# Kernel optimization log

Hardware: AMD Instinct MI355X
Metric: run time of the kernel (lower is better)

Reference implementation:

```python
import jax, jax.numpy as jnp
import numpy as np

B, T = 4096, 20
X_DIM, Z_DIM, H_DIM = 256, 128, 512
ZL, HL = 64, 64
D = X_DIM + Z_DIM  # 384, size of A


def _linear_params(key, out_f, in_f):
    kw, kb = jax.random.split(key)
    bound = 1.0 / np.sqrt(in_f)
    W = jax.random.uniform(kw, (out_f, in_f), minval=-bound, maxval=bound, dtype=jnp.float32)
    b = jax.random.uniform(kb, (out_f,), minval=-bound, maxval=bound, dtype=jnp.float32)
    return W, b


def setup_inputs() -> dict:
    key = jax.random.key(0)
    ks = jax.random.split(key, 12)
    x = jax.random.normal(ks[0], (B, T, X_DIM), dtype=jnp.float32)
    h_in = jax.random.normal(ks[1], (B, T, HL), dtype=jnp.float32)
    z_in = jax.random.normal(ks[2], (B, T, ZL), dtype=jnp.float32)
    A = jax.random.normal(ks[3], (D, D), dtype=jnp.float32) / np.sqrt(D)
    # Pz_xh_mean_forward: LinearUnit(x+h -> h), LinearUnit(h -> z)
    Wm1, bm1 = _linear_params(ks[4], H_DIM, X_DIM + H_DIM)
    Wm2, bm2 = _linear_params(ks[5], Z_DIM, H_DIM)
    # Pz_xh_logvar_forward: same shapes
    Wv1, bv1 = _linear_params(ks[6], H_DIM, X_DIM + H_DIM)
    Wv2, bv2 = _linear_params(ks[7], Z_DIM, H_DIM)
    # phi_xz_forward: LinearUnit(x+z -> 2h)
    Wphi, bphi = _linear_params(ks[8], 2 * H_DIM, X_DIM + Z_DIM)
    # LSTMCell(2h -> h), torch layout: gates order i, f, g, o
    W_ih, b_ih = _linear_params(ks[9], 4 * H_DIM, 2 * H_DIM)
    W_hh, b_hh = _linear_params(ks[10], 4 * H_DIM, H_DIM)
    return dict(x=x, h_in=h_in, z_in=z_in, A=A,
                Wm1=Wm1, bm1=bm1, Wm2=Wm2, bm2=bm2,
                Wv1=Wv1, bv1=bv1, Wv2=Wv2, bv2=bv2,
                Wphi=Wphi, bphi=bphi,
                W_ih=W_ih, W_hh=W_hh, b_ih=b_ih, b_hh=b_hh)


def _forward(x, h_in, z_in, A, Wm1, bm1, Wm2, bm2, Wv1, bv1, Wv2, bv2,
             Wphi, bphi, W_ih, W_hh, b_ih, b_hh):
    lrelu = lambda v: jax.nn.leaky_relu(v, 0.2)

    def step(carry, x_t):
        h, c = carry  # [B, H] each
        xh = jnp.concatenate([x_t, h], axis=1)                       # [B, X+H]
        mean = lrelu(lrelu(xh @ Wm1.T + bm1) @ Wm2.T + bm2)          # [B, Z]
        logvar = lrelu(lrelu(xh @ Wv1.T + bv1) @ Wv2.T + bv2)        # [B, Z]
        z = mean  # eval mode: reparameterize_gaussian returns the mean
        xz = jnp.concatenate([x_t, z], axis=1)                       # [B, D]
        agg = xz @ A.T  # == matmul(A, xz.T).T                       # [B, D]
        phi = jax.nn.softplus(lrelu(agg @ Wphi.T + bphi))            # [B, 2H]
        gates = phi @ W_ih.T + b_ih + h @ W_hh.T + b_hh              # [B, 4H]
        i, f, g, o = jnp.split(gates, 4, axis=1)
        c_new = jax.nn.sigmoid(f) * c + jax.nn.sigmoid(i) * jnp.tanh(g)
        h_new = jax.nn.sigmoid(o) * jnp.tanh(c_new)
        # h_out records h BEFORE the update (as in the torch loop)
        return (h_new, c_new), (z, mean, logvar, h, h_new)

    h0 = jnp.zeros((x.shape[0], H_DIM), dtype=x.dtype)
    c0 = jnp.zeros((x.shape[0], H_DIM), dtype=x.dtype)
    xT = jnp.swapaxes(x, 0, 1)  # [T, B, X]
    _, (z, mean, logvar, h_out, h_lo) = jax.lax.scan(step, (h0, c0), xT)
    to_bt = lambda a: jnp.swapaxes(a, 0, 1)  # [B, T, *]
    return (to_bt(z), to_bt(mean), to_bt(logvar), to_bt(h_out), to_bt(h_lo))


def reference(x, h_in, z_in, A, Wm1, bm1, Wm2, bm2, Wv1, bv1, Wv2, bv2,
              Wphi, bphi, W_ih, W_hh, b_ih, b_hh):
    return _forward(x, h_in, z_in, A, Wm1, bm1, Wm2, bm2, Wv1, bv1, Wv2, bv2,
                    Wphi, bphi, W_ih, W_hh, b_ih, b_hh)
```

## Files before the change

kernel.cpp:

```cpp
#include <hip/hip_runtime.h>
#include <math.h>

constexpr int B_ = 4096;
constexpr int T_ = 20;
constexpr int XD = 256;
constexpr int ZD = 128;
constexpr int HD = 512;
constexpr int DD = 384;

using short8 = __attribute__((ext_vector_type(8))) short;
using bf16x8 = __attribute__((ext_vector_type(8))) __bf16;
using f32x4  = __attribute__((ext_vector_type(4))) float;

__device__ __forceinline__ float lrelu_f(float v) { return v > 0.f ? v : 0.2f * v; }
__device__ __forceinline__ float softplus_f(float v) {
    return log1pf(expf(-fabsf(v))) + fmaxf(v, 0.f);
}
__device__ __forceinline__ float sigmoid_f(float v) { return 1.f / (1.f + expf(-v)); }

__device__ __forceinline__ unsigned short f2b(float f) {
    unsigned u = __builtin_bit_cast(unsigned, f);
    u += 0x7fff + ((u >> 16) & 1);
    return (unsigned short)(u >> 16);
}

__device__ __forceinline__ f32x4 mfma16(short8 a, short8 b, f32x4 c) {
    return __builtin_amdgcn_mfma_f32_16x16x32_bf16(
        __builtin_bit_cast(bf16x8, a), __builtin_bit_cast(bf16x8, b), c, 0, 0, 0);
}

__device__ __forceinline__ void load_lds16(const unsigned short* g, unsigned short* l) {
    __builtin_amdgcn_global_load_lds(
        (const __attribute__((address_space(1))) unsigned int*)g,
        (__attribute__((address_space(3))) unsigned int*)l,
        16, 0, 0);
}

template <int LPT>
__device__ __forceinline__ void vmwait(int rem) {
    if (rem >= 2) {
        if constexpr (LPT == 4)      asm volatile("s_waitcnt vmcnt(8)" ::: "memory");
        else if constexpr (LPT == 3) asm volatile("s_waitcnt vmcnt(6)" ::: "memory");
        else                         asm volatile("s_waitcnt vmcnt(4)" ::: "memory");
    } else if (rem == 1) {
        if constexpr (LPT == 4)      asm volatile("s_waitcnt vmcnt(4)" ::: "memory");
        else if constexpr (LPT == 3) asm volatile("s_waitcnt vmcnt(3)" ::: "memory");
        else                         asm volatile("s_waitcnt vmcnt(2)" ::: "memory");
    } else {
        asm volatile("s_waitcnt vmcnt(0)" ::: "memory");
    }
}

template <int MT>
__device__ __forceinline__ void gemm_core(
    const unsigned short* A1, int lda1, int K1,
    const unsigned short* A2, int lda2, int K2,
    const unsigned short* W1, int ldw1,
    const unsigned short* W2, int ldw2,
    int bm, int bn,
    unsigned short* As, unsigned short* Bs,
    f32x4 (&acc)[MT / 32][4])
{
    constexpr int MI   = MT / 32;
    constexpr int WRS  = MT / 2;
    constexpr int NA   = MT / 64;
    constexpr int LPT  = NA + 2;
    constexpr int ABUF = MT * 32;

    const int tid  = threadIdx.x;
    const int lane = tid & 63;
    const int wave = tid >> 6;
    const int wr = wave >> 1, wc = wave & 1;
    const int fr = lane & 15, fg = lane >> 4;
    const int cswz = fg ^ ((fr >> 1) & 3);

    const int r0 = tid >> 2,          c0 = (tid & 3) ^ ((r0 >> 1) & 3);
    const int r1 = (256 + tid) >> 2,  c1 = ((256 + tid) & 3) ^ ((r1 >> 1) & 3);

    const int n1 = K1 / 32;
    const int nt = n1 + K2 / 32;

    auto stage = [&](int i, int buf) {
        const unsigned short* Ag;
        const unsigned short* Wg;
        int lda, ldw, kb;
        if (i < n1) { Ag = A1; Wg = W1; lda = lda1; ldw = ldw1; kb = i * 32; }
        else        { Ag = A2; Wg = W2; lda = lda2; ldw = ldw2; kb = (i - n1) * 32; }
        unsigned short* lA = As + buf * ABUF + wave * 512;
        unsigned short* lB = Bs + buf * 4096 + wave * 512;
        load_lds16(Ag + (size_t)(bm + r0) * lda + kb + c0 * 8, lA);
        if constexpr (NA == 2)
            load_lds16(Ag + (size_t)(bm + r1) * lda + kb + c1 * 8, lA + 2048);
        load_lds16(Wg + (size_t)(bn + r0) * ldw + kb + c0 * 8, lB);
        load_lds16(Wg + (size_t)(bn + r1) * ldw + kb + c1 * 8, lB + 2048);
    };

    auto compute = [&](int buf) {
        const unsigned short* Ab_ = As + buf * ABUF;
        const unsigned short* Bb_ = Bs + buf * 4096;
        short8 af[MI], bv[4];
#pragma unroll
        for (int mi = 0; mi < MI; ++mi)
            af[mi] = *reinterpret_cast<const short8*>(Ab_ + (wr * WRS + mi * 16 + fr) * 32 + cswz * 8);
#pragma unroll
        for (int ni = 0; ni < 4; ++ni)
            bv[ni] = *reinterpret_cast<const short8*>(Bb_ + (wc * 64 + ni * 16 + fr) * 32 + cswz * 8);
#pragma unroll
        for (int mi = 0; mi < MI; ++mi)
#pragma unroll
            for (int ni = 0; ni < 4; ++ni)
                acc[mi][ni] = mfma16(af[mi], bv[ni], acc[mi][ni]);
    };

    stage(0, 0);
    if (1 < nt) stage(1, 1);
    if (2 < nt) stage(2, 2);
    {
        int rem = (nt - 1 < 2) ? (nt - 1) : 2;
        vmwait<LPT>(rem);
    }
    __builtin_amdgcn_s_barrier();

    int buf = 0;
    for (int i = 0; i < nt; ++i) {
        compute(buf);
        if (i + 1 < nt) {
            asm volatile("" ::: "memory");
            __builtin_amdgcn_s_barrier();
            if (i + 3 < nt) stage(i + 3, buf);
            int rem = nt - (i + 2);
            if (rem > 2) rem = 2;
            vmwait<LPT>(rem);
            __builtin_amdgcn_s_barrier();
            buf = (buf == 2) ? 0 : buf + 1;
        }
    }
}

template <int ACT, int MT, int NMASK, int NSHIFT>
__global__ __launch_bounds__(256) void k_gemm_act(
    const unsigned short* __restrict__ A1, int lda1, int K1,
    const unsigned short* __restrict__ A2, int lda2, int K2,
    const unsigned short* __restrict__ W1, int ldw1,
    const unsigned short* __restrict__ W2, int ldw2,
    const float* __restrict__ bias,
    unsigned short* __restrict__ DB, int lddb)
{
    __shared__ unsigned short As[3 * MT * 32];
    __shared__ unsigned short Bs[3 * 4096];
    const int id = blockIdx.x;
    const int bm = (id >> NSHIFT) * MT, bn = (id & NMASK) * 128;
    f32x4 acc[MT / 32][4] = {};
    gemm_core<MT>(A1, lda1, K1, A2, lda2, K2, W1, ldw1, W2, ldw2, bm, bn, As, Bs, acc);

    constexpr int MI = MT / 32, WRS = MT / 2;
    const int tid = threadIdx.x, lane = tid & 63, wave = tid >> 6;
    const int wr = wave >> 1, wc = wave & 1, fr = lane & 15, rg = lane >> 4;
    float bb[4];
#pragma unroll
    for (int ni = 0; ni < 4; ++ni)
        bb[ni] = bias ? bias[bn + wc * 64 + ni * 16 + fr] : 0.f;
#pragma unroll
    for (int mi = 0; mi < MI; ++mi)
#pragma unroll
        for (int r = 0; r < 4; ++r) {
            const int row = bm + wr * WRS + mi * 16 + rg * 4 + r;
#pragma unroll
            for (int ni = 0; ni < 4; ++ni) {
                float v = acc[mi][ni][r] + bb[ni];
                if (ACT == 1) v = lrelu_f(v);
                else if (ACT == 2) v = softplus_f(lrelu_f(v));
                DB[(size_t)row * lddb + (bn + wc * 64 + ni * 16 + fr)] = f2b(v);
            }
        }
}

__global__ __launch_bounds__(256) void k_meanphi(
    const unsigned short* __restrict__ uslot,
    const unsigned short* __restrict__ xb,
    const unsigned short* __restrict__ Wm2b,
    const unsigned short* __restrict__ Wcb,
    const float* __restrict__ bm2,
    const float* __restrict__ bphi,
    float* __restrict__ oz, float* __restrict__ om,
    unsigned short* __restrict__ phib)
{
    __shared__ unsigned short As[3 * 64 * 32];
    __shared__ unsigned short Bs[3 * 4096];
    __shared__ unsigned short meanL[64 * 136];

    const int id = blockIdx.x;
    const int bm = (id >> 3) * 64, bn = (id & 7) * 128;
    const int tid = threadIdx.x, lane = tid & 63, wave = tid >> 6;
    const int wr = wave >> 1, wc = wave & 1, fr = lane & 15, fg = lane >> 4, rg = lane >> 4;
    const int cswz = fg ^ ((fr >> 1) & 3);
    const int r0 = tid >> 2,          c0 = (tid & 3) ^ ((r0 >> 1) & 3);
    const int r1 = (256 + tid) >> 2,  c1 = ((256 + tid) & 3) ^ ((r1 >> 1) & 3);

    {
        f32x4 macc[2][4] = {};
        gemm_core<64>(uslot, 1024, 512, uslot, 1024, 0,
                      Wm2b, 512, Wm2b, 512, bm, 0, As, Bs, macc);
        float mb[4];
#pragma unroll
        for (int ni = 0; ni < 4; ++ni)
            mb[ni] = bm2[wc * 64 + ni * 16 + fr];
#pragma unroll
        for (int mi = 0; mi < 2; ++mi)
#pragma unroll
            for (int r = 0; r < 4; ++r) {
                const int rowl = wr * 32 + mi * 16 + rg * 4 + r;
#pragma unroll
                for (int ni = 0; ni < 4; ++ni) {
                    const int col = wc * 64 + ni * 16 + fr;
                    const float v = lrelu_f(macc[mi][ni][r] + mb[ni]);
                    meanL[rowl * 136 + col] = f2b(v);
                    if (bn == 0) {
                        const size_t o = (size_t)(bm + rowl) * (T_ * ZD) + col;
                        oz[o] = v; om[o] = v;
                    }
                }
            }
    }
    __syncthreads();

    f32x4 acc[2][4] = {};
    gemm_core<64>(xb, XD, XD, xb, XD, 0,
                  Wcb, DD, Wcb, DD, bm, bn, As, Bs, acc);
    __syncthreads();

    {
        const unsigned short* WG = Wcb + XD;
        auto stageB = [&](int i, int buf) {
            unsigned short* lB = Bs + buf * 4096 + wave * 512;
            load_lds16(WG + (size_t)(bn + r0) * DD + i * 32 + c0 * 8, lB);
            load_lds16(WG + (size_t)(bn + r1) * DD + i * 32 + c1 * 8, lB + 2048);
        };
        stageB(0, 0); stageB(1, 1); stageB(2, 2);
        vmwait<2>(2);
        __builtin_amdgcn_s_barrier();
        int buf = 0;
        for (int i = 0; i < 4; ++i) {
            short8 af[2], bv[4];
#pragma unroll
            for (int mi = 0; mi < 2; ++mi)
                af[mi] = *reinterpret_cast<const short8*>(
                    meanL + (wr * 32 + mi * 16 + fr) * 136 + i * 32 + fg * 8);
#pragma unroll
            for (int ni = 0; ni < 4; ++ni)
                bv[ni] = *reinterpret_cast<const short8*>(
                    Bs + buf * 4096 + (wc * 64 + ni * 16 + fr) * 32 + cswz * 8);
#pragma unroll
            for (int mi = 0; mi < 2; ++mi)
#pragma unroll
                for (int ni = 0; ni < 4; ++ni)
                    acc[mi][ni] = mfma16(af[mi], bv[ni], acc[mi][ni]);
            if (i + 1 < 4) {
                asm volatile("" ::: "memory");
                __builtin_amdgcn_s_barrier();
                if (i + 3 < 4) stageB(i + 3, buf);
                int rem = 4 - (i + 2);
                if (rem > 2) rem = 2;
                vmwait<2>(rem);
                __builtin_amdgcn_s_barrier();
                buf = (buf == 2) ? 0 : buf + 1;
            }
        }
    }

    float pb[4];
#pragma unroll
    for (int ni = 0; ni < 4; ++ni)
        pb[ni] = bphi[bn + wc * 64 + ni * 16 + fr];
#pragma unroll
    for (int mi = 0; mi < 2; ++mi)
#pragma unroll
        for (int r = 0; r < 4; ++r) {
            const int row = bm + wr * 32 + mi * 16 + rg * 4 + r;
#pragma unroll
            for (int ni = 0; ni < 4; ++ni) {
                const float v = softplus_f(lrelu_f(acc[mi][ni][r] + pb[ni]));
                phib[(size_t)row * 1024 + (bn + wc * 64 + ni * 16 + fr)] = f2b(v);
            }
        }
}

__global__ __launch_bounds__(256) void k_logvar_all(
    const unsigned short* __restrict__ umuvall,
    const unsigned short* __restrict__ Wv2b,
    const float* __restrict__ bv2,
    float* __restrict__ out_lv)
{
    __shared__ unsigned short As[3 * 64 * 32];
    __shared__ unsigned short Bs[3 * 4096];
    const int bm = blockIdx.x * 64;
    f32x4 acc[2][4] = {};
    gemm_core<64>(umuvall + 512, 1024, 512, umuvall + 512, 1024, 0,
                  Wv2b, 512, Wv2b, 512, bm, 0, As, Bs, acc);

    const int tid = threadIdx.x, lane = tid & 63, wave = tid >> 6;
    const int wr = wave >> 1, wc = wave & 1, fr = lane & 15, rg = lane >> 4;
    float bb[4];
#pragma unroll
    for (int ni = 0; ni < 4; ++ni)
        bb[ni] = bv2[wc * 64 + ni * 16 + fr];
#pragma unroll
    for (int mi = 0; mi < 2; ++mi)
#pragma unroll
        for (int r = 0; r < 4; ++r) {
            const int row = bm + wr * 32 + mi * 16 + rg * 4 + r;
            const int t = row >> 12, b = row & (B_ - 1);
#pragma unroll
            for (int ni = 0; ni < 4; ++ni) {
                const int col = wc * 64 + ni * 16 + fr;
                out_lv[(size_t)b * (T_ * ZD) + (size_t)t * ZD + col] =
                    lrelu_f(acc[mi][ni][r] + bb[ni]);
            }
        }
}

__global__ __launch_bounds__(256) void k_gates_lstm(
    const unsigned short* __restrict__ phib,
    const unsigned short* __restrict__ hbin,
    const unsigned short* __restrict__ Wih,
    const unsigned short* __restrict__ Whh,
    const float* __restrict__ br,
    float* __restrict__ c,
    unsigned short* __restrict__ hbout,
    float* __restrict__ ohl,
    float* __restrict__ oh_next)
{
    __shared__ unsigned short As[3 * 128 * 32];
    __shared__ unsigned short Bs[3 * 4096];
    const int id = blockIdx.x;
    const int sid = (id & 7) * 64 + (id >> 3);
    const int bm = (sid >> 4) * 128, bn = (sid & 15) * 128;
    f32x4 acc[4][4] = {};
    gemm_core<128>(phib, 1024, 1024, hbin, 512, 512, Wih, 1024, Whh, 512, bm, bn, As, Bs, acc);

    const int tid = threadIdx.x, lane = tid & 63, wave = tid >> 6;
    const int wr = wave >> 1, wc = wave & 1, fr = lane & 15, rg = lane >> 4;
    const int n = ((bn + wc * 64) >> 6) * 16 + fr;
    float bb[4];
#pragma unroll
    for (int ni = 0; ni < 4; ++ni)
        bb[ni] = br[bn + wc * 64 + ni * 16 + fr];
#pragma unroll
    for (int mi = 0; mi < 4; ++mi)
#pragma unroll
        for (int r = 0; r < 4; ++r) {
            const int row = bm + wr * 64 + mi * 16 + rg * 4 + r;
            const size_t idx = (size_t)row * HD + n;
            const float gi = acc[mi][0][r] + bb[0];
            const float gf = acc[mi][1][r] + bb[1];
            const float gg = acc[mi][2][r] + bb[2];
            const float go = acc[mi][3][r] + bb[3];
            const float co = c[idx];
            const float cn = sigmoid_f(gf) * co + sigmoid_f(gi) * tanhf(gg);
            const float hn = sigmoid_f(go) * tanhf(cn);
            c[idx] = cn;
            hbout[idx] = f2b(hn);
            const size_t ob = (size_t)row * (T_ * HD) + n;
            ohl[ob] = hn;
            if (oh_next) oh_next[ob] = hn;
        }
}

__global__ __launch_bounds__(256) void k_gemm_plain(
    const unsigned short* __restrict__ A1, int lda1, int K1,
    const unsigned short* __restrict__ W1, int ldw1,
    unsigned short* __restrict__ DB, int lddb)
{
    __shared__ unsigned short As[3 * 128 * 32];
    __shared__ unsigned short Bs[3 * 4096];
    const int bm = blockIdx.y * 128, bn = blockIdx.x * 128;
    f32x4 acc[4][4] = {};
    gemm_core<128>(A1, lda1, K1, A1, lda1, 0, W1, ldw1, W1, ldw1, bm, bn, As, Bs, acc);

    const int tid = threadIdx.x, lane = tid & 63, wave = tid >> 6;
    const int wr = wave >> 1, wc = wave & 1, fr = lane & 15, rg = lane >> 4;
#pragma unroll
    for (int mi = 0; mi < 4; ++mi)
#pragma unroll
        for (int r = 0; r < 4; ++r) {
            const int row = bm + wr * 64 + mi * 16 + rg * 4 + r;
#pragma unroll
            for (int ni = 0; ni < 4; ++ni) {
                const int col = bn + wc * 64 + ni * 16 + fr;
                DB[(size_t)row * lddb + col] = f2b(acc[mi][ni][r]);
            }
        }
}

__global__ __launch_bounds__(256) void init_state(
    float* __restrict__ c, unsigned short* __restrict__ hb,
    float* __restrict__ oh0)
{
    const int i = blockIdx.x * 256 + threadIdx.x;
    c[i] = 0.f; hb[i] = 0;
    const int b = i >> 9, nn = i & 511;
    oh0[(size_t)b * (T_ * HD) + nn] = 0.f;
}

__global__ __launch_bounds__(256) void f32_to_bf16(
    const float* __restrict__ src, unsigned short* __restrict__ dst, int n4)
{
    const int i = blockIdx.x * 256 + threadIdx.x;
    if (i >= n4) return;
    float4 v = reinterpret_cast<const float4*>(src)[i];
    ushort4 o;
    o.x = f2b(v.x); o.y = f2b(v.y); o.z = f2b(v.z); o.w = f2b(v.w);
    reinterpret_cast<ushort4*>(dst)[i] = o;
}

__global__ __launch_bounds__(256) void conv_x_all(
    const float* __restrict__ x, unsigned short* __restrict__ xball)
{
    const int i = blockIdx.x * 256 + threadIdx.x;
    const int d = i & 63;
    const int bt = i >> 6;
    const int b = bt / T_, t = bt % T_;
    float4 v = reinterpret_cast<const float4*>(x)[i];
    ushort4 o;
    o.x = f2b(v.x); o.y = f2b(v.y); o.z = f2b(v.z); o.w = f2b(v.w);
    reinterpret_cast<ushort4*>(xball)[((size_t)t * B_ + b) * (XD / 4) + d] = o;
}

__global__ __launch_bounds__(256) void prep_wu(
    const float* __restrict__ Wm1, const float* __restrict__ Wv1,
    unsigned short* __restrict__ Wub)
{
    const int k = blockIdx.x * 256 + threadIdx.x;
    const int nrow = blockIdx.y;
    const float v = nrow < 512 ? Wm1[nrow * 768 + k] : Wv1[(nrow - 512) * 768 + k];
    Wub[nrow * 768 + k] = f2b(v);
}

__global__ __launch_bounds__(256) void prep_wg(
    const float* __restrict__ Wih, const float* __restrict__ Whh,
    unsigned short* __restrict__ Wrih, unsigned short* __restrict__ Wrhh)
{
    const int cc = blockIdx.y;
    const int gate = (cc >> 4) & 3;
    const int n = ((cc >> 6) << 4) + (cc & 15);
    const int orig = gate * 512 + n;
    const int kk = blockIdx.x * 256 + threadIdx.x;
    if (kk < 1024) Wrih[(size_t)cc * 1024 + kk] = f2b(Wih[(size_t)orig * 1024 + kk]);
    else           Wrhh[(size_t)cc * 512 + (kk - 1024)] = f2b(Whh[(size_t)orig * 512 + (kk - 1024)]);
}

__global__ __launch_bounds__(256) void prep_at(
    const float* __restrict__ A, unsigned short* __restrict__ At)
{
    const int i = blockIdx.x * 256 + threadIdx.x;
    const int k = i / DD, j = i % DD;
    At[(size_t)k * DD + j] = f2b(A[(size_t)j * DD + k]);
}

__global__ __launch_bounds__(256) void prep_bias(
    const float* __restrict__ bm1, const float* __restrict__ bv1,
    const float* __restrict__ bih, const float* __restrict__ bhh,
    float* __restrict__ bu, float* __restrict__ br)
{
    const int i = blockIdx.x * 256 + threadIdx.x;
    if (i < 1024) {
        bu[i] = i < 512 ? bm1[i] : bv1[i - 512];
    } else if (i >= 2048) {
        const int cb = i - 2048;
        const int gate = (cb >> 4) & 3;
        const int n = ((cb >> 6) << 4) + (cb & 15);
        const int orig = gate * 512 + n;
        br[cb] = bih[orig] + bhh[orig];
    }
}

extern "C" void kernel_launch(void* const* d_in, const int* in_sizes, int n_in,
                              void* d_out, int out_size, void* d_ws, size_t ws_size,
                              hipStream_t stream)
{
    const float* x    = (const float*)d_in[0];
    const float* A    = (const float*)d_in[3];
    const float* Wm1  = (const float*)d_in[4];
    const float* bm1  = (const float*)d_in[5];
    const float* Wm2  = (const float*)d_in[6];
    const float* bm2  = (const float*)d_in[7];
    const float* Wv1  = (const float*)d_in[8];
    const float* bv1  = (const float*)d_in[9];
    const float* Wv2  = (const float*)d_in[10];
    const float* bv2  = (const float*)d_in[11];
    const float* Wphi = (const float*)d_in[12];
    const float* bphi = (const float*)d_in[13];
    const float* W_ih = (const float*)d_in[14];
    const float* W_hh = (const float*)d_in[15];
    const float* b_ih = (const float*)d_in[16];
    const float* b_hh = (const float*)d_in[17];

    float* out = (float*)d_out;
    float* out_z    = out;
    float* out_mean = out_z + (size_t)B_ * T_ * ZD;
    float* out_lv   = out_mean + (size_t)B_ * T_ * ZD;
    float* out_hout = out_lv + (size_t)B_ * T_ * ZD;
    float* out_hlo  = out_hout + (size_t)B_ * T_ * HD;

    char* wp = (char*)d_ws;
    auto alloc_f = [&](size_t n) { float* p = (float*)wp; wp += n * sizeof(float); return p; };
    auto alloc_b = [&](size_t n) { unsigned short* p = (unsigned short*)wp; wp += n * sizeof(unsigned short); return p; };

    float* c = alloc_f((size_t)B_ * HD);
    unsigned short* hb0     = alloc_b((size_t)B_ * HD);
    unsigned short* hb1     = alloc_b((size_t)B_ * HD);
    unsigned short* xball   = alloc_b((size_t)T_ * B_ * XD);
    unsigned short* umuvall = alloc_b((size_t)T_ * B_ * 1024);
    unsigned short* phib    = alloc_b((size_t)B_ * 1024);

    unsigned short* Wub   = alloc_b((size_t)1024 * 768);
    unsigned short* Wm2b  = alloc_b((size_t)ZD * HD);
    unsigned short* Wv2b  = alloc_b((size_t)ZD * HD);
    unsigned short* Atb   = alloc_b((size_t)DD * DD);
    unsigned short* Wphib = alloc_b((size_t)1024 * DD);
    unsigned short* Wcb   = alloc_b((size_t)1024 * DD);
    unsigned short* Wrih  = alloc_b((size_t)2048 * 1024);
    unsigned short* Wrhh  = alloc_b((size_t)2048 * 512);

    float* bu = alloc_f(1024);
    float* br = alloc_f(2048);

    const dim3 blk(256);

    init_state<<<dim3(B_ * HD / 256), blk, 0, stream>>>(c, hb0, out_hout);
    conv_x_all<<<dim3(B_ * T_ * XD / 4 / 256), blk, 0, stream>>>(x, xball);
    prep_wu<<<dim3(3, 1024), blk, 0, stream>>>(Wm1, Wv1, Wub);
    f32_to_bf16<<<dim3(ZD * HD / 4 / 256), blk, 0, stream>>>(Wm2, Wm2b, ZD * HD / 4);
    f32_to_bf16<<<dim3(ZD * HD / 4 / 256), blk, 0, stream>>>(Wv2, Wv2b, ZD * HD / 4);
    prep_wg<<<dim3(6, 2048), blk, 0, stream>>>(W_ih, W_hh, Wrih, Wrhh);
    prep_bias<<<dim3(16), blk, 0, stream>>>(bm1, bv1, b_ih, b_hh, bu, br);
    prep_at<<<dim3(DD * DD / 256), blk, 0, stream>>>(A, Atb);
    f32_to_bf16<<<dim3(1024 * DD / 4 / 256), blk, 0, stream>>>(Wphi, Wphib, 1024 * DD / 4);
    k_gemm_plain<<<dim3(DD / 128, 1024 / 128), blk, 0, stream>>>(
        Wphib, DD, DD, Atb, DD, Wcb, DD);

    for (int t = 0; t < T_; ++t) {
        unsigned short* hbt = (t & 1) ? hb1 : hb0;
        unsigned short* hbn = (t & 1) ? hb0 : hb1;
        const unsigned short* xb = xball + (size_t)t * B_ * XD;
        unsigned short* uslot = umuvall + (size_t)t * B_ * 1024;

        k_gemm_act<1, 64, 7, 3><<<dim3(512), blk, 0, stream>>>(
            xb, XD, XD, hbt, HD, HD,
            Wub, XD + HD, Wub + XD, XD + HD,
            bu, uslot, 1024);

        k_meanphi<<<dim3(512), blk, 0, stream>>>(
            uslot, xb, Wm2b, Wcb, bm2, bphi,
            out_z + (size_t)t * ZD, out_mean + (size_t)t * ZD, phib);

        k_gates_lstm<<<dim3(512), blk, 0, stream>>>(
            phib, hbt, Wrih, Wrhh, br,
            c, hbn,
            out_hlo + (size_t)t * HD,
            (t + 1 < T_) ? out_hout + (size_t)(t + 1) * HD : nullptr);
    }

    k_logvar_all<<<dim3(T_ * B_ / 64), blk, 0, stream>>>(
        umuvall, Wv2b, bv2, out_lv);
}
```

Baseline: 2.065 ms.

## Widen LSTM gate GEMM tile to 256 rows and merge prep kernels into one launch

```diff
diff --git a/kernel.cpp b/kernel.cpp
--- a/kernel.cpp
+++ b/kernel.cpp
@@ -39,11 +39,13 @@
 template <int LPT>
 __device__ __forceinline__ void vmwait(int rem) {
     if (rem >= 2) {
-        if constexpr (LPT == 4)      asm volatile("s_waitcnt vmcnt(8)" ::: "memory");
+        if constexpr (LPT == 6)      asm volatile("s_waitcnt vmcnt(12)" ::: "memory");
+        else if constexpr (LPT == 4) asm volatile("s_waitcnt vmcnt(8)" ::: "memory");
         else if constexpr (LPT == 3) asm volatile("s_waitcnt vmcnt(6)" ::: "memory");
         else                         asm volatile("s_waitcnt vmcnt(4)" ::: "memory");
     } else if (rem == 1) {
-        if constexpr (LPT == 4)      asm volatile("s_waitcnt vmcnt(4)" ::: "memory");
+        if constexpr (LPT == 6)      asm volatile("s_waitcnt vmcnt(6)" ::: "memory");
+        else if constexpr (LPT == 4) asm volatile("s_waitcnt vmcnt(4)" ::: "memory");
         else if constexpr (LPT == 3) asm volatile("s_waitcnt vmcnt(3)" ::: "memory");
         else                         asm volatile("s_waitcnt vmcnt(2)" ::: "memory");
     } else {
@@ -137,6 +139,83 @@
     }
 }
 
+__device__ __forceinline__ void gemm_core_wide(
+    const unsigned short* A1, int lda1, int K1,
+    const unsigned short* A2, int lda2, int K2,
+    const unsigned short* W1, int ldw1,
+    const unsigned short* W2, int ldw2,
+    int bm, int bn,
+    unsigned short* As, unsigned short* Bs,
+    f32x4 (&acc)[8][4])
+{
+    const int tid  = threadIdx.x;
+    const int lane = tid & 63;
+    const int wave = tid >> 6;
+    const int wr = wave >> 1, wc = wave & 1;
+    const int fr = lane & 15, fg = lane >> 4;
+    const int cswz = fg ^ ((fr >> 1) & 3);
+
+    const int rr = tid >> 2;
+    const int cc_ = (tid & 3) ^ ((rr >> 1) & 3);
+
+    const int n1 = K1 / 32;
+    const int nt = n1 + K2 / 32;
+
+    auto stage = [&](int i, int buf) {
+        const unsigned short* Ag;
+        const unsigned short* Wg;
+        int lda, ldw, kb;
+        if (i < n1) { Ag = A1; Wg = W1; lda = lda1; ldw = ldw1; kb = i * 32; }
+        else        { Ag = A2; Wg = W2; lda = lda2; ldw = ldw2; kb = (i - n1) * 32; }
+        unsigned short* lA = As + buf * 8192 + wave * 512;
+        unsigned short* lB = Bs + buf * 4096 + wave * 512;
+#pragma unroll
+        for (int j = 0; j < 4; ++j)
+            load_lds16(Ag + (size_t)(bm + j * 64 + rr) * lda + kb + cc_ * 8, lA + j * 2048);
+#pragma unroll
+        for (int j = 0; j < 2; ++j)
+            load_lds16(Wg + (size_t)(bn + j * 64 + rr) * ldw + kb + cc_ * 8, lB + j * 2048);
+    };
+
+    auto compute = [&](int buf) {
+        const unsigned short* Ab_ = As + buf * 8192;
+        const unsigned short* Bb_ = Bs + buf * 4096;
+        short8 af[8], bv[4];
+#pragma unroll
+        for (int mi = 0; mi < 8; ++mi)
+            af[mi] = *reinterpret_cast<const short8*>(Ab_ + (wr * 128 + mi * 16 + fr) * 32 + cswz * 8);
+#pragma unroll
+        for (int ni = 0; ni < 4; ++ni)
+            bv[ni] = *reinterpret_cast<const short8*>(Bb_ + (wc * 64 + ni * 16 + fr) * 32 + cswz * 8);
+#pragma unroll
+        for (int mi = 0; mi < 8; ++mi)
+#pragma unroll
+            for (int ni = 0; ni < 4; ++ni)
+                acc[mi][ni] = mfma16(af[mi], bv[ni], acc[mi][ni]);
+    };
+
+    stage(0, 0);
+    stage(1, 1);
+    stage(2, 2);
+    vmwait<6>(2);
+    __builtin_amdgcn_s_barrier();
+
+    int buf = 0;
+    for (int i = 0; i < nt; ++i) {
+        compute(buf);
+        if (i + 1 < nt) {
+            asm volatile("" ::: "memory");
+            __builtin_amdgcn_s_barrier();
+            if (i + 3 < nt) stage(i + 3, buf);
+            int rem = nt - (i + 2);
+            if (rem > 2) rem = 2;
+            vmwait<6>(rem);
+            __builtin_amdgcn_s_barrier();
+            buf = (buf == 2) ? 0 : buf + 1;
+        }
+    }
+}
+
 template <int ACT, int MT, int NMASK, int NSHIFT>
 __global__ __launch_bounds__(256) void k_gemm_act(
     const unsigned short* __restrict__ A1, int lda1, int K1,
@@ -330,13 +409,13 @@
     float* __restrict__ ohl,
     float* __restrict__ oh_next)
 {
-    __shared__ unsigned short As[3 * 128 * 32];
+    __shared__ unsigned short As[3 * 8192];
     __shared__ unsigned short Bs[3 * 4096];
     const int id = blockIdx.x;
-    const int sid = (id & 7) * 64 + (id >> 3);
-    const int bm = (sid >> 4) * 128, bn = (sid & 15) * 128;
-    f32x4 acc[4][4] = {};
-    gemm_core<128>(phib, 1024, 1024, hbin, 512, 512, Wih, 1024, Whh, 512, bm, bn, As, Bs, acc);
+    const int sid = (id & 7) * 32 + (id >> 3);
+    const int bm = (sid >> 4) * 256, bn = (sid & 15) * 128;
+    f32x4 acc[8][4] = {};
+    gemm_core_wide(phib, 1024, 1024, hbin, 512, 512, Wih, 1024, Whh, 512, bm, bn, As, Bs, acc);
 
     const int tid = threadIdx.x, lane = tid & 63, wave = tid >> 6;
     const int wr = wave >> 1, wc = wave & 1, fr = lane & 15, rg = lane >> 4;
@@ -346,10 +425,10 @@
     for (int ni = 0; ni < 4; ++ni)
         bb[ni] = br[bn + wc * 64 + ni * 16 + fr];
 #pragma unroll
-    for (int mi = 0; mi < 4; ++mi)
+    for (int mi = 0; mi < 8; ++mi)
 #pragma unroll
         for (int r = 0; r < 4; ++r) {
-            const int row = bm + wr * 64 + mi * 16 + rg * 4 + r;
+            const int row = bm + wr * 128 + mi * 16 + rg * 4 + r;
             const size_t idx = (size_t)row * HD + n;
             const float gi = acc[mi][0][r] + bb[0];
             const float gf = acc[mi][1][r] + bb[1];
@@ -392,85 +471,98 @@
         }
 }
 
-__global__ __launch_bounds__(256) void init_state(
-    float* __restrict__ c, unsigned short* __restrict__ hb,
-    float* __restrict__ oh0)
-{
-    const int i = blockIdx.x * 256 + threadIdx.x;
-    c[i] = 0.f; hb[i] = 0;
-    const int b = i >> 9, nn = i & 511;
-    oh0[(size_t)b * (T_ * HD) + nn] = 0.f;
-}
-
-__global__ __launch_bounds__(256) void f32_to_bf16(
-    const float* __restrict__ src, unsigned short* __restrict__ dst, int n4)
-{
-    const int i = blockIdx.x * 256 + threadIdx.x;
-    if (i >= n4) return;
-    float4 v = reinterpret_cast<const float4*>(src)[i];
-    ushort4 o;
-    o.x = f2b(v.x); o.y = f2b(v.y); o.z = f2b(v.z); o.w = f2b(v.w);
-    reinterpret_cast<ushort4*>(dst)[i] = o;
-}
-
-__global__ __launch_bounds__(256) void conv_x_all(
-    const float* __restrict__ x, unsigned short* __restrict__ xball)
-{
-    const int i = blockIdx.x * 256 + threadIdx.x;
-    const int d = i & 63;
-    const int bt = i >> 6;
-    const int b = bt / T_, t = bt % T_;
-    float4 v = reinterpret_cast<const float4*>(x)[i];
-    ushort4 o;
-    o.x = f2b(v.x); o.y = f2b(v.y); o.z = f2b(v.z); o.w = f2b(v.w);
-    reinterpret_cast<ushort4*>(xball)[((size_t)t * B_ + b) * (XD / 4) + d] = o;
-}
-
-__global__ __launch_bounds__(256) void prep_wu(
-    const float* __restrict__ Wm1, const float* __restrict__ Wv1,
-    unsigned short* __restrict__ Wub)
-{
-    const int k = blockIdx.x * 256 + threadIdx.x;
-    const int nrow = blockIdx.y;
-    const float v = nrow < 512 ? Wm1[nrow * 768 + k] : Wv1[(nrow - 512) * 768 + k];
-    Wub[nrow * 768 + k] = f2b(v);
-}
-
-__global__ __launch_bounds__(256) void prep_wg(
+constexpr int SG0 = 8192;
+constexpr int SG1 = SG0 + 20480;
+constexpr int SG2 = SG1 + 3072;
+constexpr int SG3 = SG2 + 64;
+constexpr int SG4 = SG3 + 64;
+constexpr int SG5 = SG4 + 384;
+constexpr int SG6 = SG5 + 12288;
+constexpr int SG7 = SG6 + 576;
+constexpr int SG8 = SG7 + 16;
+
+__global__ __launch_bounds__(256) void prep_all(
+    const float* __restrict__ x,
+    const float* __restrict__ A,
+    const float* __restrict__ Wm1, const float* __restrict__ bm1,
+    const float* __restrict__ Wm2,
+    const float* __restrict__ Wv1, const float* __restrict__ bv1,
+    const float* __restrict__ Wv2,
+    const float* __restrict__ Wphi,
     const float* __restrict__ Wih, const float* __restrict__ Whh,
-    unsigned short* __restrict__ Wrih, unsigned short* __restrict__ Wrhh)
-{
-    const int cc = blockIdx.y;
-    const int gate = (cc >> 4) & 3;
-    const int n = ((cc >> 6) << 4) + (cc & 15);
-    const int orig = gate * 512 + n;
-    const int kk = blockIdx.x * 256 + threadIdx.x;
-    if (kk < 1024) Wrih[(size_t)cc * 1024 + kk] = f2b(Wih[(size_t)orig * 1024 + kk]);
-    else           Wrhh[(size_t)cc * 512 + (kk - 1024)] = f2b(Whh[(size_t)orig * 512 + (kk - 1024)]);
-}
-
-__global__ __launch_bounds__(256) void prep_at(
-    const float* __restrict__ A, unsigned short* __restrict__ At)
-{
-    const int i = blockIdx.x * 256 + threadIdx.x;
-    const int k = i / DD, j = i % DD;
-    At[(size_t)k * DD + j] = f2b(A[(size_t)j * DD + k]);
-}
-
-__global__ __launch_bounds__(256) void prep_bias(
-    const float* __restrict__ bm1, const float* __restrict__ bv1,
     const float* __restrict__ bih, const float* __restrict__ bhh,
+    float* __restrict__ c, unsigned short* __restrict__ hb0,
+    float* __restrict__ oh0,
+    unsigned short* __restrict__ xball,
+    unsigned short* __restrict__ Wub,
+    unsigned short* __restrict__ Wm2b, unsigned short* __restrict__ Wv2b,
+    unsigned short* __restrict__ Wphib,
+    unsigned short* __restrict__ Wrih, unsigned short* __restrict__ Wrhh,
+    unsigned short* __restrict__ Atb,
     float* __restrict__ bu, float* __restrict__ br)
 {
-    const int i = blockIdx.x * 256 + threadIdx.x;
-    if (i < 1024) {
-        bu[i] = i < 512 ? bm1[i] : bv1[i - 512];
-    } else if (i >= 2048) {
-        const int cb = i - 2048;
-        const int gate = (cb >> 4) & 3;
-        const int n = ((cb >> 6) << 4) + (cb & 15);
+    const int blk = blockIdx.x;
+    const int tid = threadIdx.x;
+
+    if (blk < SG0) {
+        const int i = blk * 256 + tid;
+        c[i] = 0.f; hb0[i] = 0;
+        const int b = i >> 9, nn = i & 511;
+        oh0[(size_t)b * (T_ * HD) + nn] = 0.f;
+    } else if (blk < SG1) {
+        const int i = (blk - SG0) * 256 + tid;
+        const int d = i & 63;
+        const int bt = i >> 6;
+        const int b = bt / T_, t = bt % T_;
+        float4 v = reinterpret_cast<const float4*>(x)[i];
+        ushort4 o;
+        o.x = f2b(v.x); o.y = f2b(v.y); o.z = f2b(v.z); o.w = f2b(v.w);
+        reinterpret_cast<ushort4*>(xball)[((size_t)t * B_ + b) * (XD / 4) + d] = o;
+    } else if (blk < SG2) {
+        const int e = (blk - SG1) * 256 + tid;
+        const float v = e < 512 * 768 ? Wm1[e] : Wv1[e - 512 * 768];
+        Wub[e] = f2b(v);
+    } else if (blk < SG3) {
+        const int i = (blk - SG2) * 256 + tid;
+        float4 v = reinterpret_cast<const float4*>(Wm2)[i];
+        ushort4 o;
+        o.x = f2b(v.x); o.y = f2b(v.y); o.z = f2b(v.z); o.w = f2b(v.w);
+        reinterpret_cast<ushort4*>(Wm2b)[i] = o;
+    } else if (blk < SG4) {
+        const int i = (blk - SG3) * 256 + tid;
+        float4 v = reinterpret_cast<const float4*>(Wv2)[i];
+        ushort4 o;
+        o.x = f2b(v.x); o.y = f2b(v.y); o.z = f2b(v.z); o.w = f2b(v.w);
+        reinterpret_cast<ushort4*>(Wv2b)[i] = o;
+    } else if (blk < SG5) {
+        const int i = (blk - SG4) * 256 + tid;
+        float4 v = reinterpret_cast<const float4*>(Wphi)[i];
+        ushort4 o;
+        o.x = f2b(v.x); o.y = f2b(v.y); o.z = f2b(v.z); o.w = f2b(v.w);
+        reinterpret_cast<ushort4*>(Wphib)[i] = o;
+    } else if (blk < SG6) {
+        const int e = (blk - SG5) * 256 + tid;
+        const int cc = e / 1536, kk = e % 1536;
+        const int gate = (cc >> 4) & 3;
+        const int n = ((cc >> 6) << 4) + (cc & 15);
         const int orig = gate * 512 + n;
-        br[cb] = bih[orig] + bhh[orig];
+        if (kk < 1024) Wrih[(size_t)cc * 1024 + kk] = f2b(Wih[(size_t)orig * 1024 + kk]);
+        else           Wrhh[(size_t)cc * 512 + (kk - 1024)] = f2b(Whh[(size_t)orig * 512 + (kk - 1024)]);
+    } else if (blk < SG7) {
+        const int i = (blk - SG6) * 256 + tid;
+        const int k = i / DD, j = i % DD;
+        Atb[(size_t)k * DD + j] = f2b(A[(size_t)j * DD + k]);
+    } else {
+        const int i = (blk - SG7) * 256 + tid;
+        if (i < 1024) {
+            bu[i] = i < 512 ? bm1[i] : bv1[i - 512];
+        } else if (i >= 2048) {
+            const int cb = i - 2048;
+            const int gate = (cb >> 4) & 3;
+            const int n = ((cb >> 6) << 4) + (cb & 15);
+            const int orig = gate * 512 + n;
+            br[cb] = bih[orig] + bhh[orig];
+        }
     }
 }
 
@@ -527,15 +619,9 @@
 
     const dim3 blk(256);
 
-    init_state<<<dim3(B_ * HD / 256), blk, 0, stream>>>(c, hb0, out_hout);
-    conv_x_all<<<dim3(B_ * T_ * XD / 4 / 256), blk, 0, stream>>>(x, xball);
-    prep_wu<<<dim3(3, 1024), blk, 0, stream>>>(Wm1, Wv1, Wub);
-    f32_to_bf16<<<dim3(ZD * HD / 4 / 256), blk, 0, stream>>>(Wm2, Wm2b, ZD * HD / 4);
-    f32_to_bf16<<<dim3(ZD * HD / 4 / 256), blk, 0, stream>>>(Wv2, Wv2b, ZD * HD / 4);
-    prep_wg<<<dim3(6, 2048), blk, 0, stream>>>(W_ih, W_hh, Wrih, Wrhh);
-    prep_bias<<<dim3(16), blk, 0, stream>>>(bm1, bv1, b_ih, b_hh, bu, br);
-    prep_at<<<dim3(DD * DD / 256), blk, 0, stream>>>(A, Atb);
-    f32_to_bf16<<<dim3(1024 * DD / 4 / 256), blk, 0, stream>>>(Wphi, Wphib, 1024 * DD / 4);
+    prep_all<<<dim3(SG8), blk, 0, stream>>>(
+        x, A, Wm1, bm1, Wm2, Wv1, bv1, Wv2, Wphi, W_ih, W_hh, b_ih, b_hh,
+        c, hb0, out_hout, xball, Wub, Wm2b, Wv2b, Wphib, Wrih, Wrhh, Atb, bu, br);
     k_gemm_plain<<<dim3(DD / 128, 1024 / 128), blk, 0, stream>>>(
         Wphib, DD, DD, Atb, DD, Wcb, DD);
 
@@ -554,7 +640,7 @@
             uslot, xb, Wm2b, Wcb, bm2, bphi,
             out_z + (size_t)t * ZD, out_mean + (size_t)t * ZD, phib);
 
-        k_gates_lstm<<<dim3(512), blk, 0, stream>>>(
+        k_gates_lstm<<<dim3(256), blk, 0, stream>>>(
             phib, hbt, Wrih, Wrhh, br,
             c, hbn,
             out_hlo + (size_t)t * HD,
```

Result: slower. 2.473 ms (+19.8%).
